# Optimization experiments

Hardware: AMD Instinct MI355X
Metric: run time of the kernel (lower is better)

The kernel has to match this reference:

```python
import jax, jax.numpy as jnp
import numpy as np

B, C, H, D, HID = 1024, 64, 64, 256, 256

def setup_inputs() -> dict:
    key = jax.random.key(0)
    k1, k2, k3, k4, k5, k6, k7, k8 = jax.random.split(key, 8)
    candidate_news_vector = jax.random.normal(k1, (B, C, D), dtype=jnp.float32)
    clicked_news_vector = jax.random.normal(k2, (B, H, D), dtype=jnp.float32)
    mask_cand = jax.random.randint(k3, (B, C), 0, 2).astype(bool).at[:, 0].set(True)
    mask_hist = jax.random.randint(k4, (B, H), 0, 2).astype(bool).at[:, 0].set(True)
    # nn.Linear default init: U(-1/sqrt(fan_in), 1/sqrt(fan_in))
    s1 = 1.0 / np.sqrt(2 * D)
    s2 = 1.0 / np.sqrt(HID)
    W1 = jax.random.uniform(k5, (HID, 2 * D), minval=-s1, maxval=s1, dtype=jnp.float32)
    b1 = jax.random.uniform(k6, (HID,), minval=-s1, maxval=s1, dtype=jnp.float32)
    W2 = jax.random.uniform(k7, (1, HID), minval=-s2, maxval=s2, dtype=jnp.float32)
    b2 = jax.random.uniform(k8, (1,), minval=-s2, maxval=s2, dtype=jnp.float32)
    return {"candidate_news_vector": candidate_news_vector,
            "clicked_news_vector": clicked_news_vector,
            "mask_cand": mask_cand, "mask_hist": mask_hist,
            "W1": W1, "b1": b1, "W2": W2, "b2": b2}

def reference(candidate_news_vector, clicked_news_vector, mask_cand, mask_hist, W1, b1, W2, b2):
    d = candidate_news_vector.shape[-1]
    w2 = W2[0]                                  # [HID]
    # Two stacked Linears with no nonlinearity collapse exactly:
    # score = (W2 @ W1_c) . cand + (W2 @ W1_h) . hist + (W2 @ b1 + b2)
    v_c = W1[:, :d].T @ w2                      # [D]
    v_h = W1[:, d:].T @ w2                      # [D]
    bias = jnp.dot(w2, b1) + b2[0]
    scores = (jnp.einsum('bcd,d->bc', candidate_news_vector, v_c)[:, :, None]
              + jnp.einsum('bhd,d->bh', clicked_news_vector, v_h)[:, None, :]
              + bias)                           # [B, C, H]
    neg = jnp.finfo(scores.dtype).min
    scores = jnp.where(mask_hist[:, None, :], scores, neg)
    weights = jax.nn.softmax(scores, axis=-1)   # [B, C, H]
    weights = jnp.where(mask_cand[:, :, None], weights, 0.0)
    user_vector = jnp.einsum('bch,bhd->bcd', weights, clicked_news_vector)
    return user_vector
```

## Files before the change

### kernel.cpp

```cpp
#include <hip/hip_runtime.h>
#include <math.h>

#define NB 1024
#define NC 64
#define NH 64
#define ND 256
#define NHID 256

typedef float f4 __attribute__((ext_vector_type(4)));

#define WS_PART_OFF 1024
#define WS_UV_OFF   32768

__device__ __forceinline__ bool read_mask(const void* m, int idx, int mode) {
  if (mode == 2) return ((const float*)m)[idx] != 0.0f;
  if (mode == 1) return ((const unsigned char*)m)[idx] != 0;
  return ((const int*)m)[idx] != 0;
}

__device__ __forceinline__ void detect_mode(const unsigned int* mask_cand,
                                            const unsigned int* mask_hist,
                                            int* dst) {
  int sawf = 0; unsigned int big = 0;
  for (int i = 0; i < 32; ++i) {
    unsigned int a = mask_hist[i], b = mask_cand[i];
    if (a == 0x3f800000u || b == 0x3f800000u) sawf = 1;
    if ((a > 1u && a != 0x3f800000u) || (b > 1u && b != 0x3f800000u)) big = 1;
  }
  *dst = sawf ? 2 : (big ? 1 : 0);
}

__device__ __forceinline__ float dot4(f4 a, f4 b) {
  return fmaf(a.x, b.x, fmaf(a.y, b.y, fmaf(a.z, b.z, a.w * b.w)));
}

#define BFLY(p) { p += __shfl_xor(p, 32); p += __shfl_xor(p, 16); p += __shfl_xor(p, 8); \
                  p += __shfl_xor(p, 4);  p += __shfl_xor(p, 2);  p += __shfl_xor(p, 1); }

__global__ __launch_bounds__(256) void precompute_p1(
    const float* __restrict__ W1, const float* __restrict__ W2,
    float* __restrict__ ws)
{
  const int g = blockIdx.x;
  const int d = threadIdx.x;
  float acc = 0.f;
  #pragma unroll
  for (int jj = 0; jj < 4; ++jj) {
    int j = g * 4 + jj;
    acc = fmaf(W1[(size_t)j * (2 * ND) + ND + d], W2[j], acc);
  }
  ws[WS_PART_OFF + g * ND + d] = acc;
}

__global__ __launch_bounds__(256) void precompute_p2(
    const unsigned int* __restrict__ mask_cand,
    const unsigned int* __restrict__ mask_hist,
    float* __restrict__ ws)
{
  const int d = threadIdx.x;
  float acc = 0.f;
  #pragma unroll 8
  for (int g = 0; g < 64; ++g) acc += ws[WS_PART_OFF + g * ND + d];
  ws[d] = acc;
  if (d == 0) detect_mode(mask_cand, mask_hist, (int*)ws + ND);
}

__global__ __launch_bounds__(1024) void precompute_fallback(
    const float* __restrict__ W1, const float* __restrict__ W2,
    const unsigned int* __restrict__ mask_cand,
    const unsigned int* __restrict__ mask_hist,
    float* __restrict__ ws)
{
  __shared__ float w2_lds[NHID];
  __shared__ float partial[4][ND];
  int t = threadIdx.x;
  if (t < NHID) w2_lds[t] = W2[t];
  __syncthreads();
  int d = t & (ND - 1);
  int g = t >> 8;
  float acc = 0.f;
  #pragma unroll 8
  for (int j = g * 64; j < g * 64 + 64; ++j)
    acc = fmaf(W1[(size_t)j * (2 * ND) + ND + d], w2_lds[j], acc);
  partial[g][d] = acc;
  __syncthreads();
  if (t < ND)
    ws[t] = partial[0][t] + partial[1][t] + partial[2][t] + partial[3][t];
  if (t == 0) detect_mode(mask_cand, mask_hist, (int*)ws + ND);
}

#define LOADB(R0,R1,R2,R3,R4,R5,R6,R7, H0)                                     \
  R0 = hp4[((H0) + 0) * 64 + lane]; R1 = hp4[((H0) + 1) * 64 + lane];          \
  R2 = hp4[((H0) + 2) * 64 + lane]; R3 = hp4[((H0) + 3) * 64 + lane];          \
  R4 = hp4[((H0) + 4) * 64 + lane]; R5 = hp4[((H0) + 5) * 64 + lane];          \
  R6 = hp4[((H0) + 6) * 64 + lane]; R7 = hp4[((H0) + 7) * 64 + lane];

#define PROCB(R0,R1,R2,R3,R4,R5,R6,R7, H0)                                     \
  {                                                                            \
    float p0 = dot4(R0, vhq), p1 = dot4(R1, vhq), p2 = dot4(R2, vhq),          \
          p3 = dot4(R3, vhq), p4 = dot4(R4, vhq), p5 = dot4(R5, vhq),          \
          p6 = dot4(R6, vhq), p7 = dot4(R7, vhq);                              \
    BFLY(p0) BFLY(p1) BFLY(p2) BFLY(p3) BFLY(p4) BFLY(p5) BFLY(p6) BFLY(p7)    \
    p0 = ((mh >> ((H0) + 0)) & 1) ? p0 : -3.0e38f;                             \
    p1 = ((mh >> ((H0) + 1)) & 1) ? p1 : -3.0e38f;                             \
    p2 = ((mh >> ((H0) + 2)) & 1) ? p2 : -3.0e38f;                             \
    p3 = ((mh >> ((H0) + 3)) & 1) ? p3 : -3.0e38f;                             \
    p4 = ((mh >> ((H0) + 4)) & 1) ? p4 : -3.0e38f;                             \
    p5 = ((mh >> ((H0) + 5)) & 1) ? p5 : -3.0e38f;                             \
    p6 = ((mh >> ((H0) + 6)) & 1) ? p6 : -3.0e38f;                             \
    p7 = ((mh >> ((H0) + 7)) & 1) ? p7 : -3.0e38f;                             \
    float pm = fmaxf(fmaxf(fmaxf(p0, p1), fmaxf(p2, p3)),                      \
                     fmaxf(fmaxf(p4, p5), fmaxf(p6, p7)));                     \
    float mn = fmaxf(mrun, pm);                                                \
    float sc = expf(mrun - mn);                                                \
    float e0 = expf(p0 - mn), e1 = expf(p1 - mn), e2 = expf(p2 - mn),          \
          e3 = expf(p3 - mn), e4 = expf(p4 - mn), e5 = expf(p5 - mn),          \
          e6 = expf(p6 - mn), e7 = expf(p7 - mn);                              \
    srun = srun * sc + ((e0 + e1) + (e2 + e3)) + ((e4 + e5) + (e6 + e7));      \
    acc = acc * sc;                                                            \
    acc += e0 * R0; acc += e1 * R1; acc += e2 * R2; acc += e3 * R3;            \
    acc += e4 * R4; acc += e5 * R5; acc += e6 * R6; acc += e7 * R7;            \
    mrun = mn;                                                                 \
  }

__global__ __launch_bounds__(256, 1) void score_uv_flash(
    const float* __restrict__ hist,
    const void* __restrict__ mask_hist_v,
    const float* __restrict__ ws,
    float* __restrict__ uv_out)
{
  const int tid = threadIdx.x, lane = tid & 63, w = tid >> 6;
  const int b = blockIdx.x * 4 + w;

  const int mode = ((const int*)ws)[ND];
  const f4* hp4 = reinterpret_cast<const f4*>(hist) + (size_t)b * 4096;
  const f4 vhq = reinterpret_cast<const f4*>(ws)[lane];

  const unsigned long long mh =
      __ballot(read_mask(mask_hist_v, b * NH + lane, mode));

  float mrun = -3.0e38f, srun = 0.f;
  f4 acc = {0.f, 0.f, 0.f, 0.f};
  f4 x0, x1, x2, x3, x4, x5, x6, x7;
  f4 y0, y1, y2, y3, y4, y5, y6, y7;
  f4 z0, z1, z2, z3, z4, z5, z6, z7;
  f4 u0, u1, u2, u3, u4, u5, u6, u7;

  LOADB(x0,x1,x2,x3,x4,x5,x6,x7, 0)
  LOADB(y0,y1,y2,y3,y4,y5,y6,y7, 8)
  LOADB(z0,z1,z2,z3,z4,z5,z6,z7, 16)
  LOADB(u0,u1,u2,u3,u4,u5,u6,u7, 24)
  PROCB(x0,x1,x2,x3,x4,x5,x6,x7, 0)
  LOADB(x0,x1,x2,x3,x4,x5,x6,x7, 32)
  PROCB(y0,y1,y2,y3,y4,y5,y6,y7, 8)
  LOADB(y0,y1,y2,y3,y4,y5,y6,y7, 40)
  PROCB(z0,z1,z2,z3,z4,z5,z6,z7, 16)
  LOADB(z0,z1,z2,z3,z4,z5,z6,z7, 48)
  PROCB(u0,u1,u2,u3,u4,u5,u6,u7, 24)
  LOADB(u0,u1,u2,u3,u4,u5,u6,u7, 56)
  PROCB(x0,x1,x2,x3,x4,x5,x6,x7, 32)
  PROCB(y0,y1,y2,y3,y4,y5,y6,y7, 40)
  PROCB(z0,z1,z2,z3,z4,z5,z6,z7, 48)
  PROCB(u0,u1,u2,u3,u4,u5,u6,u7, 56)

  const f4 uv = acc * (1.0f / srun);
  reinterpret_cast<f4*>(uv_out)[b * 64 + lane] = uv;
}

__global__ __launch_bounds__(256) void broadcast_kernel(
    const float* __restrict__ uv_src,
    const void* __restrict__ mask_cand_v,
    const float* __restrict__ ws,
    float* __restrict__ out)
{
  const int bid = blockIdx.x;
  const int b = bid >> 2, q = bid & 3;
  const int t = threadIdx.x, lane = t & 63, g = t >> 6;
  const int mode = ((const int*)ws)[ND];
  const f4 uv = reinterpret_cast<const f4*>(uv_src)[b * 64 + lane];
  f4* ob4 = reinterpret_cast<f4*>(out) + (size_t)b * 4096;
  const f4 zero = {0.f, 0.f, 0.f, 0.f};
  #pragma unroll
  for (int j = 0; j < 4; ++j) {
    int c = q * 16 + g * 4 + j;
    bool mc = read_mask(mask_cand_v, b * NC + c, mode);
    f4 val = mc ? uv : zero;
    __builtin_nontemporal_store(val, &ob4[c * 64 + lane]);
  }
}

__global__ __launch_bounds__(256) void flash_fallback_kernel(
    const float* __restrict__ hist,
    const void* __restrict__ mask_cand_v,
    const void* __restrict__ mask_hist_v,
    const float* __restrict__ ws,
    float* __restrict__ out)
{
  const int tid = threadIdx.x, lane = tid & 63, w = tid >> 6;
  const int b = blockIdx.x * 4 + w;

  const int mode = ((const int*)ws)[ND];
  const f4* hp4 = reinterpret_cast<const f4*>(hist) + (size_t)b * 4096;
  const f4 vhq = reinterpret_cast<const f4*>(ws)[lane];

  const unsigned long long mh =
      __ballot(read_mask(mask_hist_v, b * NH + lane, mode));
  const unsigned long long mc =
      __ballot(read_mask(mask_cand_v, b * NC + lane, mode));

  float mrun = -3.0e38f, srun = 0.f;
  f4 acc = {0.f, 0.f, 0.f, 0.f};
  f4 x0, x1, x2, x3, x4, x5, x6, x7;
  f4 y0, y1, y2, y3, y4, y5, y6, y7;

  LOADB(x0,x1,x2,x3,x4,x5,x6,x7, 0)
  LOADB(y0,y1,y2,y3,y4,y5,y6,y7, 8)
  PROCB(x0,x1,x2,x3,x4,x5,x6,x7, 0)
  LOADB(x0,x1,x2,x3,x4,x5,x6,x7, 16)
  PROCB(y0,y1,y2,y3,y4,y5,y6,y7, 8)
  LOADB(y0,y1,y2,y3,y4,y5,y6,y7, 24)
  PROCB(x0,x1,x2,x3,x4,x5,x6,x7, 16)
  LOADB(x0,x1,x2,x3,x4,x5,x6,x7, 32)
  PROCB(y0,y1,y2,y3,y4,y5,y6,y7, 24)
  LOADB(y0,y1,y2,y3,y4,y5,y6,y7, 40)
  PROCB(x0,x1,x2,x3,x4,x5,x6,x7, 32)
  LOADB(x0,x1,x2,x3,x4,x5,x6,x7, 48)
  PROCB(y0,y1,y2,y3,y4,y5,y6,y7, 40)
  LOADB(y0,y1,y2,y3,y4,y5,y6,y7, 56)
  PROCB(x0,x1,x2,x3,x4,x5,x6,x7, 48)
  PROCB(y0,y1,y2,y3,y4,y5,y6,y7, 56)

  const f4 uv = acc * (1.0f / srun);
  const f4 zero = {0.f, 0.f, 0.f, 0.f};
  f4* ob4 = reinterpret_cast<f4*>(out) + (size_t)b * 4096;
  #pragma unroll
  for (int c = 0; c < 64; ++c)
    ob4[c * 64 + lane] = ((mc >> c) & 1ull) ? uv : zero;
}

extern "C" void kernel_launch(void* const* d_in, const int* in_sizes, int n_in,
                              void* d_out, int out_size, void* d_ws, size_t ws_size,
                              hipStream_t stream) {
  (void)in_sizes; (void)n_in; (void)out_size;
  const float* hist = (const float*)d_in[1];
  const void*  mask_cand = d_in[2];
  const void*  mask_hist = d_in[3];
  const float* W1 = (const float*)d_in[4];
  const float* W2 = (const float*)d_in[6];
  float* ws = (float*)d_ws;
  float* out = (float*)d_out;

  const bool mid = ws_size >= (size_t)(WS_PART_OFF + 64 * ND) * sizeof(float);
  const bool big = ws_size >= (size_t)(WS_UV_OFF + NB * ND) * sizeof(float);

  if (mid) {
    precompute_p1<<<64, 256, 0, stream>>>(W1, W2, ws);
    precompute_p2<<<1, 256, 0, stream>>>(
        (const unsigned int*)mask_cand, (const unsigned int*)mask_hist, ws);
  } else {
    precompute_fallback<<<1, 1024, 0, stream>>>(
        W1, W2, (const unsigned int*)mask_cand, (const unsigned int*)mask_hist, ws);
  }

  if (big) {
    score_uv_flash<<<NB / 4, 256, 0, stream>>>(hist, mask_hist, ws, ws + WS_UV_OFF);
    broadcast_kernel<<<NB * 4, 256, 0, stream>>>(ws + WS_UV_OFF, mask_cand, ws, out);
  } else {
    flash_fallback_kernel<<<NB / 4, 256, 0, stream>>>(hist, mask_cand, mask_hist, ws, out);
  }
}
```

Before: 48.17 us.

## Split history softmax across two wavefronts per batch with split-softmax merge

The score kernel now assigns two wavefronts per batch row, each handling 32 history rows. Each wave processes 8 rows at a time with 8 lanes per row, instead of one wave walking all 64 rows serially. Each half writes a partial accumulator plus its running max and sum to workspace, and the broadcast kernel merges the two halves with a log-sum-exp rescale before writing the masked output. This doubles the number of waves in flight and shortens the serial online-softmax chain, at the cost of an LDS transpose-reduction, more shuffles and a larger workspace requirement.

```diff
diff --git a/kernel.cpp b/kernel.cpp
--- a/kernel.cpp
+++ b/kernel.cpp
@@ -10,7 +10,10 @@
 typedef float f4 __attribute__((ext_vector_type(4)));
 
 #define WS_PART_OFF 1024
-#define WS_UV_OFF   32768
+#define WS_MS_OFF   20480
+#define WS_P0_OFF   32768
+#define WS_P1_OFF   (32768 + NB * ND)
+#define WS_NEED_F   (WS_P1_OFF + NB * ND)
 
 __device__ __forceinline__ bool read_mask(const void* m, int idx, int mode) {
   if (mode == 2) return ((const float*)m)[idx] != 0.0f;
@@ -87,6 +90,126 @@
   if (t < ND)
     ws[t] = partial[0][t] + partial[1][t] + partial[2][t] + partial[3][t];
   if (t == 0) detect_mode(mask_cand, mask_hist, (int*)ws + ND);
+}
+
+#define GLOAD(R0,R1,R2,R3,R4,R5,R6,R7, K)                                      \
+  {                                                                            \
+    const f4* rp_ = hb4 + ((K) * 8 + g) * 64 + sub;                            \
+    R0 = rp_[0];  R1 = rp_[8];  R2 = rp_[16]; R3 = rp_[24];                    \
+    R4 = rp_[32]; R5 = rp_[40]; R6 = rp_[48]; R7 = rp_[56];                    \
+  }
+
+#define GPROC(R0,R1,R2,R3,R4,R5,R6,R7, K)                                      \
+  {                                                                            \
+    float p = dot4(R0, vh0) + dot4(R1, vh1) + dot4(R2, vh2) + dot4(R3, vh3)    \
+            + dot4(R4, vh4) + dot4(R5, vh5) + dot4(R6, vh6) + dot4(R7, vh7);   \
+    p += __shfl_xor(p, 1); p += __shfl_xor(p, 2); p += __shfl_xor(p, 4);       \
+    const int hrow_ = half * 32 + (K) * 8 + g;                                 \
+    const bool mb_ = (mh >> hrow_) & 1ull;                                     \
+    p = mb_ ? p : -3.0e38f;                                                    \
+    float pm_ = p;                                                             \
+    pm_ = fmaxf(pm_, __shfl_xor(pm_, 8));                                      \
+    pm_ = fmaxf(pm_, __shfl_xor(pm_, 16));                                     \
+    pm_ = fmaxf(pm_, __shfl_xor(pm_, 32));                                     \
+    float mn_ = fmaxf(mrun, pm_);                                              \
+    float sc_ = expf(mrun - mn_);                                              \
+    float e_ = mb_ ? expf(p - mn_) : 0.f;                                      \
+    float ts_ = e_;                                                            \
+    ts_ += __shfl_xor(ts_, 8); ts_ += __shfl_xor(ts_, 16);                     \
+    ts_ += __shfl_xor(ts_, 32);                                                \
+    srun = srun * sc_ + ts_;                                                   \
+    a0 = a0 * sc_ + e_ * R0; a1 = a1 * sc_ + e_ * R1;                          \
+    a2 = a2 * sc_ + e_ * R2; a3 = a3 * sc_ + e_ * R3;                          \
+    a4 = a4 * sc_ + e_ * R4; a5 = a5 * sc_ + e_ * R5;                          \
+    a6 = a6 * sc_ + e_ * R6; a7 = a7 * sc_ + e_ * R7;                          \
+    mrun = mn_;                                                                \
+  }
+
+__global__ __launch_bounds__(512, 2) void score2_kernel(
+    const float* __restrict__ hist,
+    const void* __restrict__ mask_hist_v,
+    float* __restrict__ ws)
+{
+  const int t = threadIdx.x, lane = t & 63, w = t >> 6;
+  const int W = blockIdx.x * 8 + w;
+  const int b = W >> 1, half = W & 1;
+  const int sub = lane & 7, g = lane >> 3;
+
+  __shared__ f4 lds[8][64][8];
+
+  const int mode = ((const int*)ws)[ND];
+  const f4* hb4 = reinterpret_cast<const f4*>(hist)
+                + (size_t)b * 4096 + half * 32 * 64;
+  const f4* ws4 = reinterpret_cast<const f4*>(ws);
+  const f4 vh0 = ws4[sub +  0], vh1 = ws4[sub +  8];
+  const f4 vh2 = ws4[sub + 16], vh3 = ws4[sub + 24];
+  const f4 vh4 = ws4[sub + 32], vh5 = ws4[sub + 40];
+  const f4 vh6 = ws4[sub + 48], vh7 = ws4[sub + 56];
+
+  const unsigned long long mh =
+      __ballot(read_mask(mask_hist_v, b * NH + lane, mode));
+
+  float mrun = -3.0e38f, srun = 0.f;
+  f4 a0 = {0,0,0,0}, a1 = a0, a2 = a0, a3 = a0,
+     a4 = a0, a5 = a0, a6 = a0, a7 = a0;
+  f4 x0, x1, x2, x3, x4, x5, x6, x7;
+  f4 y0, y1, y2, y3, y4, y5, y6, y7;
+
+  GLOAD(x0,x1,x2,x3,x4,x5,x6,x7, 0)
+  GLOAD(y0,y1,y2,y3,y4,y5,y6,y7, 1)
+  GPROC(x0,x1,x2,x3,x4,x5,x6,x7, 0)
+  GLOAD(x0,x1,x2,x3,x4,x5,x6,x7, 2)
+  GPROC(y0,y1,y2,y3,y4,y5,y6,y7, 1)
+  GLOAD(y0,y1,y2,y3,y4,y5,y6,y7, 3)
+  GPROC(x0,x1,x2,x3,x4,x5,x6,x7, 2)
+  GPROC(y0,y1,y2,y3,y4,y5,y6,y7, 3)
+
+  lds[w][lane][0] = a0; lds[w][lane][1] = a1;
+  lds[w][lane][2] = a2; lds[w][lane][3] = a3;
+  lds[w][lane][4] = a4; lds[w][lane][5] = a5;
+  lds[w][lane][6] = a6; lds[w][lane][7] = a7;
+  asm volatile("s_waitcnt lgkmcnt(0)" ::: "memory");
+  f4 mg = {0,0,0,0};
+  #pragma unroll
+  for (int g2 = 0; g2 < 8; ++g2)
+    mg += lds[w][(lane & 7) + 8 * g2][lane >> 3];
+
+  reinterpret_cast<f4*>(ws + (half ? WS_P1_OFF : WS_P0_OFF) + b * ND)[lane] = mg;
+  if (lane == 0) {
+    ws[WS_MS_OFF + b * 4 + half * 2 + 0] = mrun;
+    ws[WS_MS_OFF + b * 4 + half * 2 + 1] = srun;
+  }
+}
+
+__global__ __launch_bounds__(256) void bcast2_kernel(
+    const void* __restrict__ mask_cand_v,
+    const float* __restrict__ ws,
+    float* __restrict__ out)
+{
+  const int bid = blockIdx.x;
+  const int b = bid >> 2, q = bid & 3;
+  const int t = threadIdx.x, lane = t & 63, g = t >> 6;
+  const int mode = ((const int*)ws)[ND];
+
+  const float m0 = ws[WS_MS_OFF + b * 4 + 0], s0 = ws[WS_MS_OFF + b * 4 + 1];
+  const float m1 = ws[WS_MS_OFF + b * 4 + 2], s1 = ws[WS_MS_OFF + b * 4 + 3];
+  const float mm = fmaxf(m0, m1);
+  const float w0 = expf(m0 - mm), w1 = expf(m1 - mm);
+  const float inv = 1.0f / (s0 * w0 + s1 * w1);
+
+  const f4 p0 = reinterpret_cast<const f4*>(ws + WS_P0_OFF + b * ND)[lane];
+  const f4 p1 = reinterpret_cast<const f4*>(ws + WS_P1_OFF + b * ND)[lane];
+  const f4 uv = (p0 * w0 + p1 * w1) * inv;
+
+  f4* ob4 = reinterpret_cast<f4*>(out) + (size_t)b * 4096;
+  const f4 zero = {0.f, 0.f, 0.f, 0.f};
+  #pragma unroll
+  for (int j = 0; j < 4; ++j) {
+    int c = q * 16 + g * 4 + j;
+    bool mc = read_mask(mask_cand_v, b * NC + c, mode);
+    f4 val = mc ? uv : zero;
+    __builtin_nontemporal_store(val, &ob4[c * 64 + lane]);
+  }
 }
 
 #define LOADB(R0,R1,R2,R3,R4,R5,R6,R7, H0)                                     \
@@ -123,72 +246,6 @@
     mrun = mn;                                                                 \
   }
 
-__global__ __launch_bounds__(256, 1) void score_uv_flash(
-    const float* __restrict__ hist,
-    const void* __restrict__ mask_hist_v,
-    const float* __restrict__ ws,
-    float* __restrict__ uv_out)
-{
-  const int tid = threadIdx.x, lane = tid & 63, w = tid >> 6;
-  const int b = blockIdx.x * 4 + w;
-
-  const int mode = ((const int*)ws)[ND];
-  const f4* hp4 = reinterpret_cast<const f4*>(hist) + (size_t)b * 4096;
-  const f4 vhq = reinterpret_cast<const f4*>(ws)[lane];
-
-  const unsigned long long mh =
-      __ballot(read_mask(mask_hist_v, b * NH + lane, mode));
-
-  float mrun = -3.0e38f, srun = 0.f;
-  f4 acc = {0.f, 0.f, 0.f, 0.f};
-  f4 x0, x1, x2, x3, x4, x5, x6, x7;
-  f4 y0, y1, y2, y3, y4, y5, y6, y7;
-  f4 z0, z1, z2, z3, z4, z5, z6, z7;
-  f4 u0, u1, u2, u3, u4, u5, u6, u7;
-
-  LOADB(x0,x1,x2,x3,x4,x5,x6,x7, 0)
-  LOADB(y0,y1,y2,y3,y4,y5,y6,y7, 8)
-  LOADB(z0,z1,z2,z3,z4,z5,z6,z7, 16)
-  LOADB(u0,u1,u2,u3,u4,u5,u6,u7, 24)
-  PROCB(x0,x1,x2,x3,x4,x5,x6,x7, 0)
-  LOADB(x0,x1,x2,x3,x4,x5,x6,x7, 32)
-  PROCB(y0,y1,y2,y3,y4,y5,y6,y7, 8)
-  LOADB(y0,y1,y2,y3,y4,y5,y6,y7, 40)
-  PROCB(z0,z1,z2,z3,z4,z5,z6,z7, 16)
-  LOADB(z0,z1,z2,z3,z4,z5,z6,z7, 48)
-  PROCB(u0,u1,u2,u3,u4,u5,u6,u7, 24)
-  LOADB(u0,u1,u2,u3,u4,u5,u6,u7, 56)
-  PROCB(x0,x1,x2,x3,x4,x5,x6,x7, 32)
-  PROCB(y0,y1,y2,y3,y4,y5,y6,y7, 40)
-  PROCB(z0,z1,z2,z3,z4,z5,z6,z7, 48)
-  PROCB(u0,u1,u2,u3,u4,u5,u6,u7, 56)
-
-  const f4 uv = acc * (1.0f / srun);
-  reinterpret_cast<f4*>(uv_out)[b * 64 + lane] = uv;
-}
-
-__global__ __launch_bounds__(256) void broadcast_kernel(
-    const float* __restrict__ uv_src,
-    const void* __restrict__ mask_cand_v,
-    const float* __restrict__ ws,
-    float* __restrict__ out)
-{
-  const int bid = blockIdx.x;
-  const int b = bid >> 2, q = bid & 3;
-  const int t = threadIdx.x, lane = t & 63, g = t >> 6;
-  const int mode = ((const int*)ws)[ND];
-  const f4 uv = reinterpret_cast<const f4*>(uv_src)[b * 64 + lane];
-  f4* ob4 = reinterpret_cast<f4*>(out) + (size_t)b * 4096;
-  const f4 zero = {0.f, 0.f, 0.f, 0.f};
-  #pragma unroll
-  for (int j = 0; j < 4; ++j) {
-    int c = q * 16 + g * 4 + j;
-    bool mc = read_mask(mask_cand_v, b * NC + c, mode);
-    f4 val = mc ? uv : zero;
-    __builtin_nontemporal_store(val, &ob4[c * 64 + lane]);
-  }
-}
-
 __global__ __launch_bounds__(256) void flash_fallback_kernel(
     const float* __restrict__ hist,
     const void* __restrict__ mask_cand_v,
@@ -251,7 +308,7 @@
   float* out = (float*)d_out;
 
   const bool mid = ws_size >= (size_t)(WS_PART_OFF + 64 * ND) * sizeof(float);
-  const bool big = ws_size >= (size_t)(WS_UV_OFF + NB * ND) * sizeof(float);
+  const bool big = ws_size >= (size_t)WS_NEED_F * sizeof(float);
 
   if (mid) {
     precompute_p1<<<64, 256, 0, stream>>>(W1, W2, ws);
@@ -263,8 +320,8 @@
   }
 
   if (big) {
-    score_uv_flash<<<NB / 4, 256, 0, stream>>>(hist, mask_hist, ws, ws + WS_UV_OFF);
-    broadcast_kernel<<<NB * 4, 256, 0, stream>>>(ws + WS_UV_OFF, mask_cand, ws, out);
+    score2_kernel<<<256, 512, 0, stream>>>(hist, mask_hist, ws);
+    bcast2_kernel<<<NB * 4, 256, 0, stream>>>(mask_cand, ws, out);
   } else {
     flash_fallback_kernel<<<NB / 4, 256, 0, stream>>>(hist, mask_cand, mask_hist, ws, out);
   }
```

After: 45.90 us. 4.7% less time.
